# Kernel optimization log

Hardware: AMD Instinct MI355X
Metric: run time of the kernel (lower is better)

## Reference

```python
import jax, jax.numpy as jnp
import numpy as np

B, T, I, H = 64, 512, 512, 1024

def setup_inputs() -> dict:
    key = jax.random.key(0)
    ks = jax.random.split(key, 12)
    s_i = 1.0 / np.sqrt(I)
    s_h = 1.0 / np.sqrt(H)
    inp = {
        'x': jax.random.normal(ks[0], (B, T, I), dtype=jnp.float32),
        'h0': jnp.zeros((B, H), dtype=jnp.float32),
        'Wz': jax.random.uniform(ks[1], (H, I), jnp.float32, -s_i, s_i),
        'bz': jax.random.uniform(ks[2], (H,), jnp.float32, -s_i, s_i),
        'Uz': jax.random.uniform(ks[3], (H, H), jnp.float32, -s_h, s_h),
        'Wr': jax.random.uniform(ks[4], (H, I), jnp.float32, -s_i, s_i),
        'br': jax.random.uniform(ks[5], (H,), jnp.float32, -s_i, s_i),
        'Ur': jax.random.uniform(ks[6], (H, H), jnp.float32, -s_h, s_h),
        'Wh': jax.random.uniform(ks[7], (H, I), jnp.float32, -s_i, s_i),
        'bh': jax.random.uniform(ks[8], (H,), jnp.float32, -s_i, s_i),
        'Uh': jax.random.uniform(ks[9], (H, H), jnp.float32, -s_h, s_h),
    }
    return inp

def reference(x, h0, Wz, bz, Uz, Wr, br, Ur, Wh, bh, Uh):
    # Precompute all input projections for every timestep in 3 big GEMMs
    xz = jnp.einsum('bti,hi->bth', x, Wz) + bz  # [B,T,H]
    xr = jnp.einsum('bti,hi->bth', x, Wr) + br
    xh = jnp.einsum('bti,hi->bth', x, Wh) + bh
    # scan over time (recurrence)
    xs = (jnp.swapaxes(xz, 0, 1), jnp.swapaxes(xr, 0, 1), jnp.swapaxes(xh, 0, 1))  # [T,B,H]

    def step(h, inp):
        xz_t, xr_t, xh_t = inp
        z = jax.nn.sigmoid(xz_t + h @ Uz.T)
        r = jax.nn.sigmoid(xr_t + h @ Ur.T)
        h_tilde = jnp.tanh(xh_t + (r * h) @ Uh.T)
        h_new = (1.0 - z) * h + z * h_tilde
        return h_new, h_new

    h_last, outs = jax.lax.scan(step, h0, xs)  # outs: [T,B,H]
    outputs = jnp.swapaxes(outs, 0, 1)  # [B,T,H]
    return outputs, h_last
```

## Files before the change

kernel.cpp:

```cpp
#include <hip/hip_runtime.h>
#include <hip/hip_bf16.h>
#include <stdint.h>


#define B_ 64
#define T_ 512
#define I_ 512
#define H_ 1024
#define NWG_A 128
#define NWG_B 64
#define NWG 192

typedef __attribute__((ext_vector_type(4))) float f32x4;
typedef __attribute__((ext_vector_type(8))) short s16x8;
typedef __attribute__((ext_vector_type(2))) unsigned int u32x2;

__device__ __forceinline__ unsigned short f2bf(float f) {
  union { float f; uint32_t u; } v; v.f = f;
  uint32_t u = v.u;
  u += 0x7fffu + ((u >> 16) & 1u);
  return (unsigned short)(u >> 16);
}
__device__ __forceinline__ float bf2f(unsigned short h) {
  union { uint32_t u; float f; } v; v.u = ((uint32_t)h) << 16;
  return v.f;
}

__device__ __forceinline__ s16x8 sc_load_b128(const uint16_t* p) {
  s16x8 r;
  asm volatile("global_load_dwordx4 %0, %1, off sc0 sc1"
               : "=v"(r) : "v"(p) : "memory");
  return r;
}
__device__ __forceinline__ float sc_load_f32(const float* p) {
  float r;
  asm volatile("global_load_dword %0, %1, off sc0 sc1"
               : "=v"(r) : "v"(p) : "memory");
  return r;
}
__device__ __forceinline__ void sc_store_f32(float* p, float v) {
  asm volatile("global_store_dword %0, %1, off sc0 sc1"
               :: "v"(p), "v"(v) : "memory");
}
__device__ __forceinline__ void sc_store_u16(uint16_t* p, unsigned v) {
  asm volatile("global_store_short %0, %1, off sc0 sc1"
               :: "v"(p), "v"(v) : "memory");
}
__device__ __forceinline__ void sc_store_u32(unsigned* p, unsigned v) {
  asm volatile("global_store_dword %0, %1, off sc0 sc1"
               :: "v"(p), "v"(v) : "memory");
}
__device__ __forceinline__ void vm_drain() {
  asm volatile("s_waitcnt vmcnt(0)" ::: "memory");
}

__global__ void k_split(const float* __restrict__ src, uint16_t* __restrict__ dst,
                        int kshift, int total) {
  int K = 1 << kshift;
  for (int i = blockIdx.x * blockDim.x + threadIdx.x; i < total;
       i += gridDim.x * blockDim.x) {
    int n = i >> kshift, k = i & (K - 1);
    float f = src[i];
    unsigned short hi = f2bf(f);
    unsigned short lo = f2bf(f - bf2f(hi));
    size_t base = (size_t)n * (3 * K);
    dst[base + k] = hi;
    dst[base + K + k] = lo;
    dst[base + 2 * K + k] = hi;
  }
}

__global__ void k_init(const float* __restrict__ h0, float* __restrict__ h,
                       uint16_t* __restrict__ h2) {
  for (int i = blockIdx.x * blockDim.x + threadIdx.x; i < B_ * H_;
       i += gridDim.x * blockDim.x) {
    float f = h0[i];
    h[i] = f;
    int b = i >> 10, j = i & 1023;
    unsigned short hi = f2bf(f);
    h2[b * 2048 + j] = hi;
    h2[b * 2048 + 1024 + j] = f2bf(f - bf2f(hi));
  }
}

__global__ __launch_bounds__(256) void k_proj(
    const float* __restrict__ x, const uint16_t* __restrict__ W2,
    const float* __restrict__ bz, const float* __restrict__ br,
    const float* __restrict__ bh,
    float* __restrict__ XP, int t0, int Tc, int MT) {
  __shared__ uint16_t As[128][72];
  __shared__ uint16_t Bs[128][72];
  int bid = blockIdx.x;
  int mt = bid % MT, nt = bid / MT;
  int tid = threadIdx.x;
  int w = tid >> 6, l = tid & 63;
  int wm = w >> 1, wn = w & 1;
  int lr = l & 15, lg = l >> 4;

  int gr[4], gc8[4];
  const float* asrc[4];
  const uint16_t* bsrc[4];
#pragma unroll
  for (int g = 0; g < 4; ++g) {
    int gran = tid + 256 * g;
    int r = gran >> 3, c8 = gran & 7;
    gr[g] = r; gc8[g] = c8;
    int n = mt * 128 + r;
    int b = n / Tc, tt = n % Tc;
    asrc[g] = x + ((size_t)b * T_ + (t0 + tt)) * I_;
    bsrc[g] = W2 + (size_t)(nt * 128 + r) * 1536;
  }

  f32x4 acc[4][4];
#pragma unroll
  for (int mi = 0; mi < 4; ++mi)
#pragma unroll
    for (int ni = 0; ni < 4; ++ni) {
      acc[mi][ni][0] = 0.f; acc[mi][ni][1] = 0.f;
      acc[mi][ni][2] = 0.f; acc[mi][ni][3] = 0.f;
    }

  float4 pa[8];
  uint4 pb[4];
#pragma unroll
  for (int g = 0; g < 4; ++g) {
    int kp = gc8[g] * 8;
    int xc = kp & 511;
    pa[2 * g] = *(const float4*)(asrc[g] + xc);
    pa[2 * g + 1] = *(const float4*)(asrc[g] + xc + 4);
    pb[g] = *(const uint4*)(bsrc[g] + kp);
  }

  for (int it = 0; it < 24; ++it) {
    __syncthreads();
    {
      int k0 = it * 64;
#pragma unroll
      for (int g = 0; g < 4; ++g) {
        int kp = k0 + gc8[g] * 8;
        bool lofl = (kp >= 1024);
        const float* pf = (const float*)&pa[2 * g];
        s16x8 v;
#pragma unroll
        for (int j = 0; j < 8; ++j) {
          float f = pf[j];
          unsigned short hi = f2bf(f);
          v[j] = (short)(lofl ? f2bf(f - bf2f(hi)) : hi);
        }
        *(s16x8*)(&As[gr[g]][gc8[g] * 8]) = v;
        *(uint4*)(&Bs[gr[g]][gc8[g] * 8]) = pb[g];
      }
    }
    if (it + 1 < 24) {
      int k0 = (it + 1) * 64;
#pragma unroll
      for (int g = 0; g < 4; ++g) {
        int kp = k0 + gc8[g] * 8;
        int xc = kp & 511;
        pa[2 * g] = *(const float4*)(asrc[g] + xc);
        pa[2 * g + 1] = *(const float4*)(asrc[g] + xc + 4);
        pb[g] = *(const uint4*)(bsrc[g] + kp);
      }
    }
    __syncthreads();
#pragma unroll
    for (int kk = 0; kk < 64; kk += 32) {
      s16x8 af[4], bf[4];
#pragma unroll
      for (int mi = 0; mi < 4; ++mi)
        af[mi] = *(const s16x8*)(&As[wm * 64 + mi * 16 + lr][kk + lg * 8]);
#pragma unroll
      for (int ni = 0; ni < 4; ++ni)
        bf[ni] = *(const s16x8*)(&Bs[wn * 64 + ni * 16 + lr][kk + lg * 8]);
#pragma unroll
      for (int mi = 0; mi < 4; ++mi)
#pragma unroll
        for (int ni = 0; ni < 4; ++ni)
          acc[mi][ni] = __builtin_amdgcn_mfma_f32_16x16x32_bf16(
              af[mi], bf[ni], acc[mi][ni], 0, 0, 0);
    }
  }

  int g_ = (nt * 128) >> 10;
  const float* bias = (g_ == 0) ? bz : ((g_ == 1) ? br : bh);
#pragma unroll
  for (int ni = 0; ni < 4; ++ni) {
    int col = nt * 128 + wn * 64 + ni * 16 + lr;
    int jc = col & 1023;
    float bv = bias[jc];
#pragma unroll
    for (int mi = 0; mi < 4; ++mi) {
      int nrow = mt * 128 + wm * 64 + mi * 16 + lg * 4;
      int b = nrow / Tc, tt = nrow % Tc;
#pragma unroll
      for (int v = 0; v < 4; ++v) {
        XP[((size_t)((tt * 3 + g_) * 64 + b)) * 1024 + jc] = acc[mi][ni][v] + bv;
        if (++tt == Tc) { tt = 0; ++b; }
      }
    }
  }
}

__global__ __launch_bounds__(512) void k_recur(
    const float* __restrict__ Uz, const float* __restrict__ Ur,
    const float* __restrict__ Uh, const float* __restrict__ XP,
    int t0i, int Tcc, float* __restrict__ h, uint16_t* __restrict__ h2,
    uint16_t* __restrict__ s2, float* __restrict__ zbuf,
    float* __restrict__ out, unsigned* __restrict__ flagsA,
    unsigned* __restrict__ flagsB) {
  __shared__ uint16_t Wl[16 * 3072];
  __shared__ float red[8 * 64 * 17];

  const int tid = threadIdx.x;
  const int w = tid >> 6, l = tid & 63;
  const int lr = l & 15, lg = l >> 4;
  const int bid = blockIdx.x;
  const bool isA = (bid < NWG_A);
  const int tile = isA ? bid : (bid - NWG_A);
  const int n0 = tile * 16;
  const bool isR = isA && (n0 >= 1024);

  const float* src = isA ? ((n0 < 1024) ? (Uz + (size_t)n0 * 1024)
                                        : (Ur + (size_t)(n0 - 1024) * 1024))
                         : (Uh + (size_t)n0 * 1024);
  for (int i = tid; i < 2048; i += 512) {
    int r = i >> 7;
    int k8 = (i & 127) * 8;
    const float* p = src + r * 1024 + k8;
    s16x8 hi8, lo8;
#pragma unroll
    for (int j = 0; j < 8; ++j) {
      float f = p[j];
      unsigned short hb = f2bf(f);
      hi8[j] = (short)hb;
      lo8[j] = (short)f2bf(f - bf2f(hb));
    }
    uint8_t* rowp = (uint8_t*)Wl + r * 6144;
    int swz = (r & 7) << 4;
    *(s16x8*)(rowp + ((k8 * 2) ^ swz)) = hi8;
    *(s16x8*)(rowp + (((1024 + k8) * 2) ^ swz)) = lo8;
    *(s16x8*)(rowp + (((2048 + k8) * 2) ^ swz)) = hi8;
  }
  __syncthreads();

  const int KB0 = w * 128;
  const int bswz = (lr & 7) << 4;
  const uint8_t* browp = (const uint8_t*)Wl + lr * 6144;

  int eb[2], ec[2];
#pragma unroll
  for (int u = 0; u < 2; ++u) {
    int e = tid + u * 512;
    eb[u] = e >> 4; ec[u] = e & 15;
  }

  float hreg[2];
  if (!isA) {
#pragma unroll
    for (int u = 0; u < 2; ++u)
      hreg[u] = h[eb[u] * 1024 + (n0 + ec[u])];
  }

  for (int tt = 0; tt < Tcc; ++tt) {
    const unsigned t = (unsigned)(t0i + tt);

    float xpre[2];
    {
      int gate = isA ? (isR ? 1 : 0) : 2;
#pragma unroll
      for (int u = 0; u < 2; ++u) {
        int jc = (n0 + ec[u]) & 1023;
        xpre[u] = XP[((size_t)(tt * 3 + gate) * 64 + eb[u]) * 1024 + jc];
      }
    }

    if (isA) {
      if (t > 0 && w == 0) {
        const unsigned* fp = flagsB + l;
        for (;;) {
          unsigned f;
          asm volatile("global_load_dword %0, %1, off sc0 sc1\n\t"
                       "s_waitcnt vmcnt(0)"
                       : "=v"(f) : "v"(fp) : "memory");
          if (__all(f >= t)) break;
        }
      }
      __syncthreads();

      float hpre[2];
      if (isR) {
#pragma unroll
        for (int u = 0; u < 2; ++u)
          hpre[u] = sc_load_f32(h + eb[u] * 1024 + (n0 - 1024 + ec[u]));
      }

      s16x8 ah[4][4], al[4][4];
#pragma unroll
      for (int ks = 0; ks < 4; ++ks)
#pragma unroll
        for (int mi = 0; mi < 4; ++mi)
          ah[ks][mi] = sc_load_b128(h2 + (size_t)(lr + 16 * mi) * 2048 +
                                    (KB0 + ks * 32 + lg * 8));
#pragma unroll
      for (int ks = 0; ks < 4; ++ks)
#pragma unroll
        for (int mi = 0; mi < 4; ++mi)
          al[ks][mi] = sc_load_b128(h2 + (size_t)(lr + 16 * mi) * 2048 +
                                    (1024 + KB0 + ks * 32 + lg * 8));

      f32x4 acc[4];
#pragma unroll
      for (int mi = 0; mi < 4; ++mi) {
        acc[mi][0] = 0.f; acc[mi][1] = 0.f; acc[mi][2] = 0.f; acc[mi][3] = 0.f;
      }

      asm volatile("s_waitcnt vmcnt(16)" ::: "memory");
      __builtin_amdgcn_sched_barrier(0);
#pragma unroll
      for (int ks = 0; ks < 4; ++ks) {
        int kp = KB0 + ks * 32 + lg * 8;
        s16x8 bfv = *(const s16x8*)(browp + ((kp * 2) ^ bswz));
#pragma unroll
        for (int mi = 0; mi < 4; ++mi)
          acc[mi] = __builtin_amdgcn_mfma_f32_16x16x32_bf16(ah[ks][mi], bfv,
                                                            acc[mi], 0, 0, 0);
      }
#pragma unroll
      for (int ks = 0; ks < 4; ++ks) {
        int kp = 1024 + KB0 + ks * 32 + lg * 8;
        s16x8 bfv = *(const s16x8*)(browp + ((kp * 2) ^ bswz));
#pragma unroll
        for (int mi = 0; mi < 4; ++mi)
          acc[mi] = __builtin_amdgcn_mfma_f32_16x16x32_bf16(ah[ks][mi], bfv,
                                                            acc[mi], 0, 0, 0);
      }
      vm_drain();
      __builtin_amdgcn_sched_barrier(0);
#pragma unroll
      for (int ks = 0; ks < 4; ++ks) {
        int kp = 2048 + KB0 + ks * 32 + lg * 8;
        s16x8 bfv = *(const s16x8*)(browp + ((kp * 2) ^ bswz));
#pragma unroll
        for (int mi = 0; mi < 4; ++mi)
          acc[mi] = __builtin_amdgcn_mfma_f32_16x16x32_bf16(al[ks][mi], bfv,
                                                            acc[mi], 0, 0, 0);
      }
#pragma unroll
      for (int mi = 0; mi < 4; ++mi)
#pragma unroll
        for (int v = 0; v < 4; ++v)
          red[(w * 64 + mi * 16 + lg * 4 + v) * 17 + lr] = acc[mi][v];
      __syncthreads();

#pragma unroll
      for (int u = 0; u < 2; ++u) {
        int b = eb[u], c = ec[u];
        float s = 0.f;
#pragma unroll
        for (int q = 0; q < 8; ++q) s += red[(q * 64 + b) * 17 + c];
        float pre = s + xpre[u];
        if (!isR) {
          int n = n0 + c;
          sc_store_f32(zbuf + b * 1024 + n, 1.f / (1.f + __expf(-pre)));
        } else {
          int j = n0 - 1024 + c;
          float r = 1.f / (1.f + __expf(-pre));
          float sv = r * hpre[u];
          unsigned short hb = f2bf(sv);
          sc_store_u16(s2 + b * 2048 + j, hb);
          sc_store_u16(s2 + b * 2048 + 1024 + j, f2bf(sv - bf2f(hb)));
        }
      }
      vm_drain();
      __syncthreads();
      if (tid == 0) sc_store_u32(flagsA + tile, t + 1);
    } else {
      if (w == 0) {
        const u32x2* fp = (const u32x2*)flagsA + l;
        unsigned tgt = t + 1;
        for (;;) {
          u32x2 f;
          asm volatile("global_load_dwordx2 %0, %1, off sc0 sc1\n\t"
                       "s_waitcnt vmcnt(0)"
                       : "=v"(f) : "v"(fp) : "memory");
          if (__all((f.x >= tgt) && (f.y >= tgt))) break;
        }
      }
      __syncthreads();

      float zpre[2];
#pragma unroll
      for (int u = 0; u < 2; ++u)
        zpre[u] = sc_load_f32(zbuf + eb[u] * 1024 + (n0 + ec[u]));

      s16x8 ah[4][4], al[4][4];
#pragma unroll
      for (int ks = 0; ks < 4; ++ks)
#pragma unroll
        for (int mi = 0; mi < 4; ++mi)
          ah[ks][mi] = sc_load_b128(s2 + (size_t)(lr + 16 * mi) * 2048 +
                                    (KB0 + ks * 32 + lg * 8));
#pragma unroll
      for (int ks = 0; ks < 4; ++ks)
#pragma unroll
        for (int mi = 0; mi < 4; ++mi)
          al[ks][mi] = sc_load_b128(s2 + (size_t)(lr + 16 * mi) * 2048 +
                                    (1024 + KB0 + ks * 32 + lg * 8));

      f32x4 acc[4];
#pragma unroll
      for (int mi = 0; mi < 4; ++mi) {
        acc[mi][0] = 0.f; acc[mi][1] = 0.f; acc[mi][2] = 0.f; acc[mi][3] = 0.f;
      }

      asm volatile("s_waitcnt vmcnt(16)" ::: "memory");
      __builtin_amdgcn_sched_barrier(0);
#pragma unroll
      for (int ks = 0; ks < 4; ++ks) {
        int kp = KB0 + ks * 32 + lg * 8;
        s16x8 bfv = *(const s16x8*)(browp + ((kp * 2) ^ bswz));
#pragma unroll
        for (int mi = 0; mi < 4; ++mi)
          acc[mi] = __builtin_amdgcn_mfma_f32_16x16x32_bf16(ah[ks][mi], bfv,
                                                            acc[mi], 0, 0, 0);
      }
#pragma unroll
      for (int ks = 0; ks < 4; ++ks) {
        int kp = 1024 + KB0 + ks * 32 + lg * 8;
        s16x8 bfv = *(const s16x8*)(browp + ((kp * 2) ^ bswz));
#pragma unroll
        for (int mi = 0; mi < 4; ++mi)
          acc[mi] = __builtin_amdgcn_mfma_f32_16x16x32_bf16(ah[ks][mi], bfv,
                                                            acc[mi], 0, 0, 0);
      }
      vm_drain();
      __builtin_amdgcn_sched_barrier(0);
#pragma unroll
      for (int ks = 0; ks < 4; ++ks) {
        int kp = 2048 + KB0 + ks * 32 + lg * 8;
        s16x8 bfv = *(const s16x8*)(browp + ((kp * 2) ^ bswz));
#pragma unroll
        for (int mi = 0; mi < 4; ++mi)
          acc[mi] = __builtin_amdgcn_mfma_f32_16x16x32_bf16(al[ks][mi], bfv,
                                                            acc[mi], 0, 0, 0);
      }
#pragma unroll
      for (int mi = 0; mi < 4; ++mi)
#pragma unroll
        for (int v = 0; v < 4; ++v)
          red[(w * 64 + mi * 16 + lg * 4 + v) * 17 + lr] = acc[mi][v];
      __syncthreads();

#pragma unroll
      for (int u = 0; u < 2; ++u) {
        int b = eb[u], c = ec[u];
        float s = 0.f;
#pragma unroll
        for (int q = 0; q < 8; ++q) s += red[(q * 64 + b) * 17 + c];
        int j = n0 + c;
        float pre = s + xpre[u];
        float ht = tanhf(pre);
        float z = zpre[u];
        float hv = hreg[u];
        float hn = (1.f - z) * hv + z * ht;
        hreg[u] = hn;
        sc_store_f32(h + b * 1024 + j, hn);
        unsigned short hb = f2bf(hn);
        sc_store_u16(h2 + b * 2048 + j, hb);
        sc_store_u16(h2 + b * 2048 + 1024 + j, f2bf(hn - bf2f(hb)));
        out[((size_t)b * T_ + (t0i + tt)) * 1024 + j] = hn;
        if (t0i + tt == T_ - 1)
          out[(size_t)B_ * T_ * 1024 + b * 1024 + j] = hn;
      }
      vm_drain();
      __syncthreads();
      if (tid == 0) sc_store_u32(flagsB + tile, t + 1);
    }
  }
}

extern "C" void kernel_launch(void* const* d_in, const int* in_sizes, int n_in,
                              void* d_out, int out_size, void* d_ws, size_t ws_size,
                              hipStream_t stream) {
  const float* x  = (const float*)d_in[0];
  const float* h0 = (const float*)d_in[1];
  const float* Wz = (const float*)d_in[2];
  const float* bz = (const float*)d_in[3];
  const float* Uz = (const float*)d_in[4];
  const float* Wr = (const float*)d_in[5];
  const float* br = (const float*)d_in[6];
  const float* Ur = (const float*)d_in[7];
  const float* Wh = (const float*)d_in[8];
  const float* bh = (const float*)d_in[9];
  const float* Uh = (const float*)d_in[10];
  float* out = (float*)d_out;

  uint8_t* ws = (uint8_t*)d_ws;
  uint16_t* W2    = (uint16_t*)(ws + 0);
  float*    hbuf  = (float*)   (ws + 9437184);
  uint16_t* h2    = (uint16_t*)(ws + 9699328);
  uint16_t* s2    = (uint16_t*)(ws + 9961472);
  float*    zbuf  = (float*)   (ws + 10223616);
  unsigned* flagsA= (unsigned*)(ws + 10485760);
  unsigned* flagsB= (unsigned*)(ws + 10486272);
  float*    XP    = (float*)   (ws + 10489856);

  hipMemsetAsync((void*)flagsA, 0, 1024, stream);

  k_split<<<512, 256, 0, stream>>>(Wz, W2, 9, 1024 * 512);
  k_split<<<512, 256, 0, stream>>>(Wr, W2 + (size_t)1024 * 1536, 9, 1024 * 512);
  k_split<<<512, 256, 0, stream>>>(Wh, W2 + (size_t)2048 * 1536, 9, 1024 * 512);
  k_init<<<64, 256, 0, stream>>>(h0, hbuf, h2);

  size_t avail = (ws_size > 10489856u) ? (ws_size - 10489856u) : 0u;
  long long tcl = (long long)(avail / 786432u);
  int Tc = (tcl > 512) ? 512 : (int)tcl;
  Tc &= ~1;
  if (Tc < 2) Tc = 2;

  for (int t0 = 0; t0 < T_; t0 += Tc) {
    int Tcc = (Tc < T_ - t0) ? Tc : (T_ - t0);
    int MT = (B_ * Tcc) / 128;
    k_proj<<<MT * 24, 256, 0, stream>>>(x, W2, bz, br, bh, XP, t0, Tcc, MT);

    int t0v = t0, tccv = Tcc;
    void* args[] = {(void*)&Uz, (void*)&Ur, (void*)&Uh, (void*)&XP,
                    (void*)&t0v, (void*)&tccv, (void*)&hbuf, (void*)&h2,
                    (void*)&s2, (void*)&zbuf, (void*)&out,
                    (void*)&flagsA, (void*)&flagsB};
    hipLaunchCooperativeKernel((void*)k_recur, dim3(NWG), dim3(512),
                               args, 0, stream);
  }
}
```

Baseline: 17.38 ms.

## Pad sync flags, relax h-state load coherence, and shrink LDS weight copy

Each per-workgroup flag is padded to its own 256-byte slot so spinning waiters do not contend on shared cache lines, and the spin loops now sleep briefly between polls and finish with an agent-scope acquire load. The loads of the recurrent state switch from sc0 sc1 to sc0 only, so they may be served from the L2 cache instead of bypassing it. The duplicated hi copy of the weights in LDS is removed and the hi fragments are kept in registers for reuse in the lo pass, shrinking LDS and cutting LDS reads. The risks are stale reads if the relaxed loads are not properly ordered after the acquire, and extra latency from the sleep.

```diff
diff --git a/kernel.cpp b/kernel.cpp
--- a/kernel.cpp
+++ b/kernel.cpp
@@ -10,10 +10,10 @@
 #define NWG_A 128
 #define NWG_B 64
 #define NWG 192
+#define FSTR 64
 
 typedef __attribute__((ext_vector_type(4))) float f32x4;
 typedef __attribute__((ext_vector_type(8))) short s16x8;
-typedef __attribute__((ext_vector_type(2))) unsigned int u32x2;
 
 __device__ __forceinline__ unsigned short f2bf(float f) {
   union { float f; uint32_t u; } v; v.f = f;
@@ -26,18 +26,6 @@
   return v.f;
 }
 
-__device__ __forceinline__ s16x8 sc_load_b128(const uint16_t* p) {
-  s16x8 r;
-  asm volatile("global_load_dwordx4 %0, %1, off sc0 sc1"
-               : "=v"(r) : "v"(p) : "memory");
-  return r;
-}
-__device__ __forceinline__ float sc_load_f32(const float* p) {
-  float r;
-  asm volatile("global_load_dword %0, %1, off sc0 sc1"
-               : "=v"(r) : "v"(p) : "memory");
-  return r;
-}
 __device__ __forceinline__ void sc_store_f32(float* p, float v) {
   asm volatile("global_store_dword %0, %1, off sc0 sc1"
                :: "v"(p), "v"(v) : "memory");
@@ -49,6 +37,18 @@
 __device__ __forceinline__ void sc_store_u32(unsigned* p, unsigned v) {
   asm volatile("global_store_dword %0, %1, off sc0 sc1"
                :: "v"(p), "v"(v) : "memory");
+}
+__device__ __forceinline__ s16x8 sc0_load_b128(const uint16_t* p) {
+  s16x8 r;
+  asm volatile("global_load_dwordx4 %0, %1, off sc0"
+               : "=v"(r) : "v"(p) : "memory");
+  return r;
+}
+__device__ __forceinline__ float sc0_load_f32(const float* p) {
+  float r;
+  asm volatile("global_load_dword %0, %1, off sc0"
+               : "=v"(r) : "v"(p) : "memory");
+  return r;
 }
 __device__ __forceinline__ void vm_drain() {
   asm volatile("s_waitcnt vmcnt(0)" ::: "memory");
@@ -208,7 +208,7 @@
     uint16_t* __restrict__ s2, float* __restrict__ zbuf,
     float* __restrict__ out, unsigned* __restrict__ flagsA,
     unsigned* __restrict__ flagsB) {
-  __shared__ uint16_t Wl[16 * 3072];
+  __shared__ uint16_t Wl[16 * 2048];
   __shared__ float red[8 * 64 * 17];
 
   const int tid = threadIdx.x;
@@ -235,17 +235,16 @@
       hi8[j] = (short)hb;
       lo8[j] = (short)f2bf(f - bf2f(hb));
     }
-    uint8_t* rowp = (uint8_t*)Wl + r * 6144;
+    uint8_t* rowp = (uint8_t*)Wl + r * 4096;
     int swz = (r & 7) << 4;
     *(s16x8*)(rowp + ((k8 * 2) ^ swz)) = hi8;
     *(s16x8*)(rowp + (((1024 + k8) * 2) ^ swz)) = lo8;
-    *(s16x8*)(rowp + (((2048 + k8) * 2) ^ swz)) = hi8;
   }
   __syncthreads();
 
   const int KB0 = w * 128;
   const int bswz = (lr & 7) << 4;
-  const uint8_t* browp = (const uint8_t*)Wl + lr * 6144;
+  const uint8_t* browp = (const uint8_t*)Wl + lr * 4096;
 
   int eb[2], ec[2];
 #pragma unroll
@@ -276,14 +275,19 @@
 
     if (isA) {
       if (t > 0 && w == 0) {
-        const unsigned* fp = flagsB + l;
+        const unsigned* fp = flagsB + (size_t)l * FSTR;
         for (;;) {
           unsigned f;
           asm volatile("global_load_dword %0, %1, off sc0 sc1\n\t"
                        "s_waitcnt vmcnt(0)"
                        : "=v"(f) : "v"(fp) : "memory");
           if (__all(f >= t)) break;
+          __builtin_amdgcn_s_sleep(4);
         }
+        if (l == 0)
+          (void)__hip_atomic_load(flagsB, __ATOMIC_ACQUIRE,
+                                  __HIP_MEMORY_SCOPE_AGENT);
+        vm_drain();
       }
       __syncthreads();
 
@@ -291,7 +295,7 @@
       if (isR) {
 #pragma unroll
         for (int u = 0; u < 2; ++u)
-          hpre[u] = sc_load_f32(h + eb[u] * 1024 + (n0 - 1024 + ec[u]));
+          hpre[u] = sc0_load_f32(h + eb[u] * 1024 + (n0 - 1024 + ec[u]));
       }
 
       s16x8 ah[4][4], al[4][4];
@@ -299,14 +303,14 @@
       for (int ks = 0; ks < 4; ++ks)
 #pragma unroll
         for (int mi = 0; mi < 4; ++mi)
-          ah[ks][mi] = sc_load_b128(h2 + (size_t)(lr + 16 * mi) * 2048 +
-                                    (KB0 + ks * 32 + lg * 8));
+          ah[ks][mi] = sc0_load_b128(h2 + (size_t)(lr + 16 * mi) * 2048 +
+                                     (KB0 + ks * 32 + lg * 8));
 #pragma unroll
       for (int ks = 0; ks < 4; ++ks)
 #pragma unroll
         for (int mi = 0; mi < 4; ++mi)
-          al[ks][mi] = sc_load_b128(h2 + (size_t)(lr + 16 * mi) * 2048 +
-                                    (1024 + KB0 + ks * 32 + lg * 8));
+          al[ks][mi] = sc0_load_b128(h2 + (size_t)(lr + 16 * mi) * 2048 +
+                                     (1024 + KB0 + ks * 32 + lg * 8));
 
       f32x4 acc[4];
 #pragma unroll
@@ -316,35 +320,33 @@
 
       asm volatile("s_waitcnt vmcnt(16)" ::: "memory");
       __builtin_amdgcn_sched_barrier(0);
+      s16x8 bfv0[4];
 #pragma unroll
       for (int ks = 0; ks < 4; ++ks) {
         int kp = KB0 + ks * 32 + lg * 8;
-        s16x8 bfv = *(const s16x8*)(browp + ((kp * 2) ^ bswz));
+        bfv0[ks] = *(const s16x8*)(browp + ((kp * 2) ^ bswz));
+#pragma unroll
+        for (int mi = 0; mi < 4; ++mi)
+          acc[mi] = __builtin_amdgcn_mfma_f32_16x16x32_bf16(ah[ks][mi], bfv0[ks],
+                                                            acc[mi], 0, 0, 0);
+      }
+#pragma unroll
+      for (int ks = 0; ks < 4; ++ks) {
+        int kp = KB0 + ks * 32 + lg * 8;
+        s16x8 bfv = *(const s16x8*)(browp + (((1024 + kp) * 2) ^ bswz));
 #pragma unroll
         for (int mi = 0; mi < 4; ++mi)
           acc[mi] = __builtin_amdgcn_mfma_f32_16x16x32_bf16(ah[ks][mi], bfv,
                                                             acc[mi], 0, 0, 0);
       }
-#pragma unroll
-      for (int ks = 0; ks < 4; ++ks) {
-        int kp = 1024 + KB0 + ks * 32 + lg * 8;
-        s16x8 bfv = *(const s16x8*)(browp + ((kp * 2) ^ bswz));
-#pragma unroll
-        for (int mi = 0; mi < 4; ++mi)
-          acc[mi] = __builtin_amdgcn_mfma_f32_16x16x32_bf16(ah[ks][mi], bfv,
-                                                            acc[mi], 0, 0, 0);
-      }
       vm_drain();
       __builtin_amdgcn_sched_barrier(0);
 #pragma unroll
-      for (int ks = 0; ks < 4; ++ks) {
-        int kp = 2048 + KB0 + ks * 32 + lg * 8;
-        s16x8 bfv = *(const s16x8*)(browp + ((kp * 2) ^ bswz));
-#pragma unroll
-        for (int mi = 0; mi < 4; ++mi)
-          acc[mi] = __builtin_amdgcn_mfma_f32_16x16x32_bf16(al[ks][mi], bfv,
+      for (int ks = 0; ks < 4; ++ks)
+#pragma unroll
+        for (int mi = 0; mi < 4; ++mi)
+          acc[mi] = __builtin_amdgcn_mfma_f32_16x16x32_bf16(al[ks][mi], bfv0[ks],
                                                             acc[mi], 0, 0, 0);
-      }
 #pragma unroll
       for (int mi = 0; mi < 4; ++mi)
 #pragma unroll
@@ -373,39 +375,46 @@
       }
       vm_drain();
       __syncthreads();
-      if (tid == 0) sc_store_u32(flagsA + tile, t + 1);
+      if (tid == 0) sc_store_u32(flagsA + (size_t)tile * FSTR, t + 1);
     } else {
       if (w == 0) {
-        const u32x2* fp = (const u32x2*)flagsA + l;
+        const unsigned* fp0 = flagsA + (size_t)(2 * l) * FSTR;
+        const unsigned* fp1 = flagsA + (size_t)(2 * l + 1) * FSTR;
         unsigned tgt = t + 1;
         for (;;) {
-          u32x2 f;
-          asm volatile("global_load_dwordx2 %0, %1, off sc0 sc1\n\t"
+          unsigned f0, f1;
+          asm volatile("global_load_dword %0, %2, off sc0 sc1\n\t"
+                       "global_load_dword %1, %3, off sc0 sc1\n\t"
                        "s_waitcnt vmcnt(0)"
-                       : "=v"(f) : "v"(fp) : "memory");
-          if (__all((f.x >= tgt) && (f.y >= tgt))) break;
+                       : "=v"(f0), "=v"(f1) : "v"(fp0), "v"(fp1) : "memory");
+          if (__all((f0 >= tgt) && (f1 >= tgt))) break;
+          __builtin_amdgcn_s_sleep(4);
         }
+        if (l == 0)
+          (void)__hip_atomic_load(flagsA, __ATOMIC_ACQUIRE,
+                                  __HIP_MEMORY_SCOPE_AGENT);
+        vm_drain();
       }
       __syncthreads();
 
       float zpre[2];
 #pragma unroll
       for (int u = 0; u < 2; ++u)
-        zpre[u] = sc_load_f32(zbuf + eb[u] * 1024 + (n0 + ec[u]));
+        zpre[u] = sc0_load_f32(zbuf + eb[u] * 1024 + (n0 + ec[u]));
 
       s16x8 ah[4][4], al[4][4];
 #pragma unroll
       for (int ks = 0; ks < 4; ++ks)
 #pragma unroll
         for (int mi = 0; mi < 4; ++mi)
-          ah[ks][mi] = sc_load_b128(s2 + (size_t)(lr + 16 * mi) * 2048 +
-                                    (KB0 + ks * 32 + lg * 8));
+          ah[ks][mi] = sc0_load_b128(s2 + (size_t)(lr + 16 * mi) * 2048 +
+                                     (KB0 + ks * 32 + lg * 8));
 #pragma unroll
       for (int ks = 0; ks < 4; ++ks)
 #pragma unroll
         for (int mi = 0; mi < 4; ++mi)
-          al[ks][mi] = sc_load_b128(s2 + (size_t)(lr + 16 * mi) * 2048 +
-                                    (1024 + KB0 + ks * 32 + lg * 8));
+          al[ks][mi] = sc0_load_b128(s2 + (size_t)(lr + 16 * mi) * 2048 +
+                                     (1024 + KB0 + ks * 32 + lg * 8));
 
       f32x4 acc[4];
 #pragma unroll
@@ -415,35 +424,33 @@
 
       asm volatile("s_waitcnt vmcnt(16)" ::: "memory");
       __builtin_amdgcn_sched_barrier(0);
+      s16x8 bfv0[4];
 #pragma unroll
       for (int ks = 0; ks < 4; ++ks) {
         int kp = KB0 + ks * 32 + lg * 8;
-        s16x8 bfv = *(const s16x8*)(browp + ((kp * 2) ^ bswz));
+        bfv0[ks] = *(const s16x8*)(browp + ((kp * 2) ^ bswz));
+#pragma unroll
+        for (int mi = 0; mi < 4; ++mi)
+          acc[mi] = __builtin_amdgcn_mfma_f32_16x16x32_bf16(ah[ks][mi], bfv0[ks],
+                                                            acc[mi], 0, 0, 0);
+      }
+#pragma unroll
+      for (int ks = 0; ks < 4; ++ks) {
+        int kp = KB0 + ks * 32 + lg * 8;
+        s16x8 bfv = *(const s16x8*)(browp + (((1024 + kp) * 2) ^ bswz));
 #pragma unroll
         for (int mi = 0; mi < 4; ++mi)
           acc[mi] = __builtin_amdgcn_mfma_f32_16x16x32_bf16(ah[ks][mi], bfv,
                                                             acc[mi], 0, 0, 0);
       }
-#pragma unroll
-      for (int ks = 0; ks < 4; ++ks) {
-        int kp = 1024 + KB0 + ks * 32 + lg * 8;
-        s16x8 bfv = *(const s16x8*)(browp + ((kp * 2) ^ bswz));
-#pragma unroll
-        for (int mi = 0; mi < 4; ++mi)
-          acc[mi] = __builtin_amdgcn_mfma_f32_16x16x32_bf16(ah[ks][mi], bfv,
-                                                            acc[mi], 0, 0, 0);
-      }
       vm_drain();
       __builtin_amdgcn_sched_barrier(0);
 #pragma unroll
-      for (int ks = 0; ks < 4; ++ks) {
-        int kp = 2048 + KB0 + ks * 32 + lg * 8;
-        s16x8 bfv = *(const s16x8*)(browp + ((kp * 2) ^ bswz));
-#pragma unroll
-        for (int mi = 0; mi < 4; ++mi)
-          acc[mi] = __builtin_amdgcn_mfma_f32_16x16x32_bf16(al[ks][mi], bfv,
+      for (int ks = 0; ks < 4; ++ks)
+#pragma unroll
+        for (int mi = 0; mi < 4; ++mi)
+          acc[mi] = __builtin_amdgcn_mfma_f32_16x16x32_bf16(al[ks][mi], bfv0[ks],
                                                             acc[mi], 0, 0, 0);
-      }
 #pragma unroll
       for (int mi = 0; mi < 4; ++mi)
 #pragma unroll
@@ -468,13 +475,13 @@
         unsigned short hb = f2bf(hn);
         sc_store_u16(h2 + b * 2048 + j, hb);
         sc_store_u16(h2 + b * 2048 + 1024 + j, f2bf(hn - bf2f(hb)));
-        out[((size_t)b * T_ + (t0i + tt)) * 1024 + j] = hn;
+        sc_store_f32(out + ((size_t)b * T_ + (t0i + tt)) * 1024 + j, hn);
         if (t0i + tt == T_ - 1)
-          out[(size_t)B_ * T_ * 1024 + b * 1024 + j] = hn;
+          sc_store_f32(out + (size_t)B_ * T_ * 1024 + b * 1024 + j, hn);
       }
       vm_drain();
       __syncthreads();
-      if (tid == 0) sc_store_u32(flagsB + tile, t + 1);
+      if (tid == 0) sc_store_u32(flagsB + (size_t)tile * FSTR, t + 1);
     }
   }
 }
@@ -502,17 +509,17 @@
   uint16_t* s2    = (uint16_t*)(ws + 9961472);
   float*    zbuf  = (float*)   (ws + 10223616);
   unsigned* flagsA= (unsigned*)(ws + 10485760);
-  unsigned* flagsB= (unsigned*)(ws + 10486272);
-  float*    XP    = (float*)   (ws + 10489856);
-
-  hipMemsetAsync((void*)flagsA, 0, 1024, stream);
+  unsigned* flagsB= (unsigned*)(ws + 10518528);
+  float*    XP    = (float*)   (ws + 10534912);
+
+  hipMemsetAsync((void*)flagsA, 0, 49152, stream);
 
   k_split<<<512, 256, 0, stream>>>(Wz, W2, 9, 1024 * 512);
   k_split<<<512, 256, 0, stream>>>(Wr, W2 + (size_t)1024 * 1536, 9, 1024 * 512);
   k_split<<<512, 256, 0, stream>>>(Wh, W2 + (size_t)2048 * 1536, 9, 1024 * 512);
   k_init<<<64, 256, 0, stream>>>(h0, hbuf, h2);
 
-  size_t avail = (ws_size > 10489856u) ? (ws_size - 10489856u) : 0u;
+  size_t avail = (ws_size > 10534912u) ? (ws_size - 10534912u) : 0u;
   long long tcl = (long long)(avail / 786432u);
   int Tc = (tcl > 512) ? 512 : (int)tcl;
   Tc &= ~1;
```

New measurement: 15.89 ms. -8.6%, faster.
